# Kernel tuning notes

Hardware: AMD Instinct MI355X
Metric: run time of the kernel (lower is better)

The kernel has to match this reference:

```python
import jax, jax.numpy as jnp
import numpy as np
import math

L, D, H, V, B, S, MR = 8, 768, 12, 32000, 2, 1024, 4
HD = D // H

def setup_inputs() -> dict:
    key = jax.random.key(0)
    ks = iter(jax.random.split(key, 64))
    def rn(shape, s=0.02):
        return jax.random.normal(next(ks), shape, jnp.float32) * s
    inp = {}
    inp['tokens'] = jax.random.randint(next(ks), (B, S), 0, V, jnp.int32)
    inp['tok_emb'] = rn((V, D))
    inp['pos_emb'] = rn((S, D))
    for n in ['Wq_row', 'Wk_row', 'Wv_row', 'Wq_col', 'Wo']:
        inp[n] = rn((L, D, D))
    for n in ['bq_row', 'bk_row', 'bv_row', 'bq_col', 'bo']:
        inp[n] = jnp.zeros((L, D), jnp.float32)
    inp['ln1_g'] = jnp.ones((L, D), jnp.float32); inp['ln1_b'] = jnp.zeros((L, D), jnp.float32)
    inp['ln2_g'] = jnp.ones((L, D), jnp.float32); inp['ln2_b'] = jnp.zeros((L, D), jnp.float32)
    inp['W1'] = rn((L, D, MR * D)); inp['b1'] = jnp.zeros((L, MR * D), jnp.float32)
    inp['W2'] = rn((L, MR * D, D)); inp['b2'] = jnp.zeros((L, D), jnp.float32)
    inp['Wk_sh'] = rn((D, D)); inp['bk_sh'] = jnp.zeros((D,), jnp.float32)
    inp['Wv_sh'] = rn((D, D)); inp['bv_sh'] = jnp.zeros((D,), jnp.float32)
    inp['lnf_g'] = jnp.ones((D,), jnp.float32); inp['lnf_b'] = jnp.zeros((D,), jnp.float32)
    inp['Whead'] = rn((D, V)); inp['bhead'] = jnp.zeros((V,), jnp.float32)
    return inp

def _ln(x, g, b, eps=1e-5):
    m = x.mean(-1, keepdims=True)
    v = ((x - m) ** 2).mean(-1, keepdims=True)
    return (x - m) * jax.lax.rsqrt(v + eps) * g + b

def _heads(x):
    b, s, _ = x.shape
    return x.reshape(b, s, H, HD).transpose(0, 2, 1, 3)  # [B,H,S,hd]

def _merge(x):
    b, h, s, hd = x.shape
    return x.transpose(0, 2, 1, 3).reshape(b, s, h * hd)

def _forward(tokens, tok_emb, pos_emb, Wq_row, bq_row, Wk_row, bk_row, Wv_row, bv_row,
             Wq_col, bq_col, Wo, bo, ln1_g, ln1_b, ln2_g, ln2_b, W1, b1, W2, b2,
             Wk_sh, bk_sh, Wv_sh, bv_sh, lnf_g, lnf_b, Whead, bhead):
    s_len = tokens.shape[1]
    inv = 1.0 / math.sqrt(HD)
    x = tok_emb[tokens] + pos_emb[:s_len]
    mask = jnp.triu(jnp.ones((s_len, s_len), bool), 1)
    past_k, past_v = [], []
    for i in range(L):
        h = _ln(x, ln1_g[i], ln1_b[i])
        q_row = _heads(h @ Wq_row[i] + bq_row[i])
        k_row = _heads(h @ Wk_row[i] + bk_row[i])
        v_row = _heads(h @ Wv_row[i] + bv_row[i])
        q_col = _heads(h @ Wq_col[i] + bq_col[i])
        k_col = _heads(h @ Wk_sh + bk_sh)   # shared KV projector (archived memory)
        v_col = _heads(h @ Wv_sh + bv_sh)
        ts = jnp.einsum('bhqd,bhkd->bhqk', q_row, k_row) * inv
        ts = jnp.where(mask, -jnp.inf, ts)
        if past_k:
            pk = jnp.stack(past_k, axis=3)  # [B,H,S,l,hd]
            pv = jnp.stack(past_v, axis=3)
            ms = jnp.einsum('bhsd,bhsld->bhsl', q_col, pk) * inv
            w = jax.nn.softmax(jnp.concatenate([ts, ms], axis=-1), axis=-1)
            tw, mw = w[..., :s_len], w[..., s_len:]
            ctx = (jnp.einsum('bhqk,bhkd->bhqd', tw, v_row)
                   + jnp.einsum('bhsl,bhsld->bhsd', mw, pv))
        else:
            ctx = jnp.einsum('bhqk,bhkd->bhqd', jax.nn.softmax(ts, axis=-1), v_row)
        x = x + (_merge(ctx) @ Wo[i] + bo[i])
        h2 = _ln(x, ln2_g[i], ln2_b[i])
        x = x + (jax.nn.gelu(h2 @ W1[i] + b1[i], approximate=False) @ W2[i] + b2[i])
        past_k.append(k_col)
        past_v.append(v_col)
    return _ln(x, lnf_g, lnf_b) @ Whead + bhead

def reference(tokens, tok_emb, pos_emb, Wq_row, bq_row, Wk_row, bk_row, Wv_row, bv_row,
              Wq_col, bq_col, Wo, bo, ln1_g, ln1_b, ln2_g, ln2_b, W1, b1, W2, b2,
              Wk_sh, bk_sh, Wv_sh, bv_sh, lnf_g, lnf_b, Whead, bhead):
    return _forward(tokens, tok_emb, pos_emb, Wq_row, bq_row, Wk_row, bk_row, Wv_row, bv_row,
                    Wq_col, bq_col, Wo, bo, ln1_g, ln1_b, ln2_g, ln2_b, W1, b1, W2, b2,
                    Wk_sh, bk_sh, Wv_sh, bv_sh, lnf_g, lnf_b, Whead, bhead)
```

## Files before the change

### kernel.cpp

```cpp
#include <hip/hip_runtime.h>
#include <hip/hip_bf16.h>
#include <math.h>

#define L_   8
#define D_   768
#define H_   12
#define V_   32000
#define B_   2
#define S_   1024
#define HD_  64
#define BS_  2048
#define DFF_ 3072

typedef __hip_bfloat16 bf16;
typedef __attribute__((ext_vector_type(8))) short bf16x8;
typedef __attribute__((ext_vector_type(4))) float f32x4;

#define CFUN(r) (((r) >> 1) & 3)

__device__ __forceinline__ void cp16(void* lds, const void* g) {
  __builtin_amdgcn_global_load_lds(
      (const __attribute__((address_space(1))) void*)g,
      (__attribute__((address_space(3))) void*)lds, 16, 0, 0);
}

__device__ __forceinline__ unsigned short f2bf(float v) {
  __hip_bfloat16 h = __float2bfloat16(v);
  return *reinterpret_cast<unsigned short*>(&h);
}
__device__ __forceinline__ float bf2f(unsigned short u) {
  return __uint_as_float(((unsigned)u) << 16);
}

__global__ __launch_bounds__(256) void k_embed(const int* __restrict__ tokens,
    const float* __restrict__ tok_emb, const float* __restrict__ pos_emb,
    float* __restrict__ x) {
  int idx = blockIdx.x * 256 + threadIdx.x;
  int row = idx / D_;
  int d   = idx - row * D_;
  int s   = row & (S_ - 1);
  int t   = tokens[row];
  x[idx] = tok_emb[(size_t)t * D_ + d] + pos_emb[(size_t)s * D_ + d];
}

__global__ __launch_bounds__(256) void k_ln(const float* __restrict__ x,
    const float* __restrict__ g, const float* __restrict__ b,
    bf16* __restrict__ out) {
  int row = blockIdx.x;
  const float* xr = x + (size_t)row * D_;
  int t = threadIdx.x;
  float v0 = xr[t], v1 = xr[t + 256], v2 = xr[t + 512];
  float s  = v0 + v1 + v2;
  float s2 = v0 * v0 + v1 * v1 + v2 * v2;
#pragma unroll
  for (int off = 32; off; off >>= 1) {
    s  += __shfl_down(s, off);
    s2 += __shfl_down(s2, off);
  }
  __shared__ float rs[4], rs2[4];
  __shared__ float mean_s, rstd_s;
  int wid = t >> 6;
  if ((t & 63) == 0) { rs[wid] = s; rs2[wid] = s2; }
  __syncthreads();
  if (t == 0) {
    float S1 = rs[0] + rs[1] + rs[2] + rs[3];
    float S2 = rs2[0] + rs2[1] + rs2[2] + rs2[3];
    float m  = S1 / D_;
    float var = S2 / D_ - m * m;
    mean_s = m;
    rstd_s = rsqrtf(var + 1e-5f);
  }
  __syncthreads();
  float m = mean_s, r = rstd_s;
  bf16* orow = out + (size_t)row * D_;
  orow[t]       = __float2bfloat16((v0 - m) * r * g[t]       + b[t]);
  orow[t + 256] = __float2bfloat16((v1 - m) * r * g[t + 256] + b[t + 256]);
  orow[t + 512] = __float2bfloat16((v2 - m) * r * g[t + 512] + b[t + 512]);
}

__global__ __launch_bounds__(256) void k_w2bf_t(const float* __restrict__ W,
    bf16* __restrict__ Wt, int K, int N, size_t ils, size_t ols) {
  __shared__ float t[32][33];
  const float* Wm = W + (size_t)blockIdx.z * ils;
  bf16* Wtm = Wt + (size_t)blockIdx.z * ols;
  int n0 = blockIdx.x * 32, k0 = blockIdx.y * 32;
  int tx = threadIdx.x;
  for (int i = threadIdx.y; i < 32; i += 8)
    t[i][tx] = Wm[(size_t)(k0 + i) * N + n0 + tx];
  __syncthreads();
  for (int i = threadIdx.y; i < 32; i += 8)
    Wtm[(size_t)(n0 + i) * K + k0 + tx] = __float2bfloat16(t[tx][i]);
}

__global__ __launch_bounds__(256) void k_bcat(const float* __restrict__ bq,
    const float* __restrict__ bk, const float* __restrict__ bqc,
    const float* __restrict__ bv, const float* __restrict__ bksh,
    const float* __restrict__ bvsh, float* __restrict__ b6) {
  int idx = blockIdx.x * 256 + threadIdx.x;
  if (idx >= L_ * 4608) return;
  int l = idx / 4608, c = idx - l * 4608;
  float v = (c < 768)  ? bq[l * 768 + c]
          : (c < 1536) ? bk[l * 768 + c - 768]
          : (c < 2304) ? bqc[l * 768 + c - 1536]
          : (c < 3072) ? bv[l * 768 + c - 2304]
          : (c < 3840) ? bksh[c - 3072]
                       : bvsh[c - 3840];
  b6[idx] = v;
}

template <int BM, int EPI>
__global__ __launch_bounds__(256) void k_bgemm(
    const bf16* __restrict__ A, const bf16* __restrict__ Wt,
    const float* __restrict__ bias, const float* __restrict__ resid,
    float* __restrict__ Cf, bf16* __restrict__ Cb, bf16* __restrict__ Cb2,
    bf16* __restrict__ Cb3, int NM, int M, int N, int K) {
  constexpr int ASZ = BM * 64;
  constexpr int ALINES = BM / 64;
  constexpr int BSTRIDE = ASZ + 8192;
  constexpr int MF = BM / 32;
  __shared__ __align__(16) char smem[3 * BSTRIDE];
  const int tid = threadIdx.x;
  const int l = tid & 63, w = tid >> 6;
  const int wr = w >> 1, wc = w & 1;

  const int nwg = (int)gridDim.x;
  int id = (int)blockIdx.x;
  id = (id & 7) * (nwg >> 3) + (id >> 3);
  const int m0 = (id % NM) * BM;
  const int n0 = (id / NM) * 128;

  const int lane15 = l & 15, lg = l >> 4;

  const int r0 = tid >> 2, p0 = tid & 3;
  const char* aSrc[ALINES];
#pragma unroll
  for (int i = 0; i < ALINES; i++) {
    const int rr = i * 64 + r0;
    aSrc[i] = (const char*)(A + (size_t)(m0 + rr) * K) + ((p0 ^ CFUN(rr)) * 16);
  }
  const char* bSrc0 = (const char*)(Wt + (size_t)(n0 + r0) * K) + ((p0 ^ CFUN(r0)) * 16);
  const char* bSrc1 = (const char*)(Wt + (size_t)(n0 + 64 + r0) * K) + ((p0 ^ CFUN(64 + r0)) * 16);

  int aOff[MF], bOff[4];
#pragma unroll
  for (int mi = 0; mi < MF; mi++) {
    int r = wr * (BM / 2) + mi * 16 + lane15;
    aOff[mi] = r * 64 + ((lg ^ CFUN(r)) * 16);
  }
#pragma unroll
  for (int ni = 0; ni < 4; ni++) {
    int r = wc * 64 + ni * 16 + lane15;
    bOff[ni] = ASZ + r * 64 + ((lg ^ CFUN(r)) * 16);
  }

  f32x4 acc[MF][4];
#pragma unroll
  for (int mi = 0; mi < MF; mi++)
#pragma unroll
    for (int ni = 0; ni < 4; ni++) acc[mi][ni] = (f32x4){0.f, 0.f, 0.f, 0.f};

  auto stage = [&](int buf, int t) {
    const size_t kb = (size_t)t * 64;
    char* base = smem + buf * BSTRIDE;
#pragma unroll
    for (int i = 0; i < ALINES; i++)
      cp16(base + i * 4096 + w * 1024, aSrc[i] + kb);
    cp16(base + ASZ + w * 1024, bSrc0 + kb);
    cp16(base + ASZ + 4096 + w * 1024, bSrc1 + kb);
  };
  auto compute = [&](int buf) {
    const char* base = smem + buf * BSTRIDE;
    bf16x8 af[MF], bfr[4];
#pragma unroll
    for (int mi = 0; mi < MF; mi++) af[mi] = *(const bf16x8*)(base + aOff[mi]);
#pragma unroll
    for (int ni = 0; ni < 4; ni++) bfr[ni] = *(const bf16x8*)(base + bOff[ni]);
    __builtin_amdgcn_s_setprio(1);
#pragma unroll
    for (int mi = 0; mi < MF; mi++)
#pragma unroll
      for (int ni = 0; ni < 4; ni++)
        acc[mi][ni] = __builtin_amdgcn_mfma_f32_16x16x32_bf16(
            af[mi], bfr[ni], acc[mi][ni], 0, 0, 0);
    __builtin_amdgcn_s_setprio(0);
  };

  const int nk = K >> 5;
  stage(0, 0);
  stage(1, 1);
  int buf = 0;
  for (int t = 0; t < nk; t++) {
    if (t + 1 < nk) {
      if constexpr (ALINES == 2) asm volatile("s_waitcnt vmcnt(4)" ::: "memory");
      else                       asm volatile("s_waitcnt vmcnt(3)" ::: "memory");
    } else {
      asm volatile("s_waitcnt vmcnt(0)" ::: "memory");
    }
    __builtin_amdgcn_s_barrier();
    if (t + 2 < nk) {
      int nb = buf + 2; if (nb >= 3) nb -= 3;
      stage(nb, t + 2);
    }
    compute(buf);
    buf = (buf == 2) ? 0 : buf + 1;
  }

#pragma unroll
  for (int ni = 0; ni < 4; ni++) {
    const int col = n0 + wc * 64 + ni * 16 + lane15;
    const float bv = bias[col];
#pragma unroll
    for (int mi = 0; mi < MF; mi++) {
      const int rowb = m0 + wr * (BM / 2) + mi * 16 + lg * 4;
      if constexpr (EPI == 6) {
        if (col < 2304) {
#pragma unroll
          for (int j = 0; j < 4; j++)
            Cb[(size_t)(rowb + j) * 2304 + col] = __float2bfloat16(acc[mi][ni][j] + bv);
        } else if (col < 3072) {
          ushort4 pk;
          pk.x = f2bf(acc[mi][ni][0] + bv);
          pk.y = f2bf(acc[mi][ni][1] + bv);
          pk.z = f2bf(acc[mi][ni][2] + bv);
          pk.w = f2bf(acc[mi][ni][3] + bv);
          const int bq = rowb >> 10, s = rowb & (S_ - 1);
          *reinterpret_cast<ushort4*>(
              (unsigned short*)Cb2 + ((size_t)(bq * 768 + (col - 2304))) * S_ + s) = pk;
        } else {
#pragma unroll
          for (int j = 0; j < 4; j++)
            Cb3[(size_t)(rowb + j) * 1536 + (col - 3072)] =
                __float2bfloat16(acc[mi][ni][j] + bv);
        }
      } else {
#pragma unroll
        for (int j = 0; j < 4; j++) {
          const int row = rowb + j;
          float v = acc[mi][ni][j] + bv;
          if constexpr (EPI == 1) v += resid[(size_t)row * N + col];
          if constexpr (EPI == 2) {
            v = 0.5f * v * (1.0f + erff(v * 0.70710678118654752f));
            Cb[(size_t)row * N + col] = __float2bfloat16(v);
          } else if constexpr (EPI == 3) {
            Cb[(size_t)row * N + col] = __float2bfloat16(v);
          } else {
            Cf[(size_t)row * N + col] = v;
          }
        }
      }
    }
  }
}

#define HBAR() asm volatile("s_barrier" ::: "memory")
#define MFMA16(AF, BF, MB, NB)                                               \
  do {                                                                       \
    __builtin_amdgcn_s_setprio(1);                                           \
    _Pragma("unroll") for (int mi_ = 0; mi_ < 4; mi_++)                      \
      _Pragma("unroll") for (int ni_ = 0; ni_ < 2; ni_++)                    \
        _Pragma("unroll") for (int ks_ = 0; ks_ < 2; ks_++)                  \
          acc[(MB) + mi_][(NB) + ni_] =                                      \
              __builtin_amdgcn_mfma_f32_16x16x32_bf16(                       \
                  AF[mi_][ks_], BF[ni_][ks_], acc[(MB) + mi_][(NB) + ni_],   \
                  0, 0, 0);                                                  \
    __builtin_amdgcn_s_setprio(0);                                           \
  } while (0)

__global__ __launch_bounds__(512, 1) void k_head8(const bf16* __restrict__ A,
    const bf16* __restrict__ Wt, const float* __restrict__ bias,
    float* __restrict__ C) {
  __shared__ __align__(16) char smem[131072];
  const int tid = threadIdx.x;
  const int l = tid & 63, w = tid >> 6;
  const int wr = w >> 2, wc = w & 3;
  const int lane15 = l & 15, lg = l >> 4;

  int id = (int)blockIdx.x;
  id = (id & 7) * 125 + (id >> 3);
  const int m0 = (id % 8) * 256;
  const int n0 = (id / 8) * 256;

  auto issueA = [&](int tile, int hb) {
#pragma unroll
    for (int j = 0; j < 2; j++) {
      const int idx = j * 512 + tid;
      const int rl = idx >> 3, sl = idx & 7;
      const bf16* g = A + (size_t)(m0 + hb + rl) * 768 + tile * 64 +
                      ((sl ^ (rl & 7)) << 3);
      cp16(smem + (tile & 1) * 32768 + hb * 128 + (j * 512 + w * 64) * 16, g);
    }
  };
  auto issueB = [&](int tile, int hb) {
#pragma unroll
    for (int j = 0; j < 2; j++) {
      const int idx = j * 512 + tid;
      const int rl = idx >> 3, sl = idx & 7;
      const bf16* g = Wt + (size_t)(n0 + hb + rl) * 768 + tile * 64 +
                      ((sl ^ (rl & 7)) << 3);
      cp16(smem + 65536 + (tile & 1) * 32768 + hb * 128 + (j * 512 + w * 64) * 16, g);
    }
  };
  auto ldA = [&](int buf, int mi, int ks) {
    const int r = wr * 128 + mi * 16 + lane15;
    return *(const bf16x8*)(smem + buf * 32768 + r * 128 +
                            ((((ks << 2) + lg) ^ (r & 7)) << 4));
  };
  auto ldB = [&](int buf, int ni, int ks) {
    const int r = wc * 64 + ni * 16 + lane15;
    return *(const bf16x8*)(smem + 65536 + buf * 32768 + r * 128 +
                            ((((ks << 2) + lg) ^ (r & 7)) << 4));
  };

  f32x4 acc[8][4];
#pragma unroll
  for (int i = 0; i < 8; i++)
#pragma unroll
    for (int j = 0; j < 4; j++) acc[i][j] = (f32x4){0.f, 0.f, 0.f, 0.f};
  bf16x8 alo[4][2], ahi[4][2], blo[2][2], bhi[2][2];

  issueA(0, 0);  issueA(0, 128);  issueB(0, 0);  issueB(0, 128);
  issueB(1, 0);  issueA(1, 0);    issueB(1, 128);
  asm volatile("s_waitcnt vmcnt(6)" ::: "memory");
  HBAR();

  for (int it = 0; it < 5; ++it) {
    const int Tb = 2 * it + 1, Tn = 2 * it + 2;
#pragma unroll
    for (int mi = 0; mi < 4; mi++) { alo[mi][0] = ldA(0, mi, 0); alo[mi][1] = ldA(0, mi, 1); }
#pragma unroll
    for (int ni = 0; ni < 2; ni++) { blo[ni][0] = ldB(0, ni, 0); blo[ni][1] = ldB(0, ni, 1); }
    issueA(Tb, 128);
    HBAR(); MFMA16(alo, blo, 0, 0); HBAR();
#pragma unroll
    for (int ni = 0; ni < 2; ni++) { bhi[ni][0] = ldB(0, ni + 2, 0); bhi[ni][1] = ldB(0, ni + 2, 1); }
    HBAR(); MFMA16(alo, bhi, 0, 2); HBAR();
#pragma unroll
    for (int mi = 0; mi < 4; mi++) { ahi[mi][0] = ldA(0, mi + 4, 0); ahi[mi][1] = ldA(0, mi + 4, 1); }
    issueB(Tn, 0);
    HBAR(); MFMA16(ahi, bhi, 4, 2); HBAR();
    issueA(Tn, 0);
    issueB(Tn, 128);
    asm volatile("s_waitcnt vmcnt(6)" ::: "memory");
    HBAR(); MFMA16(ahi, blo, 4, 0); HBAR();
#pragma unroll
    for (int mi = 0; mi < 4; mi++) { alo[mi][0] = ldA(1, mi, 0); alo[mi][1] = ldA(1, mi, 1); }
#pragma unroll
    for (int ni = 0; ni < 2; ni++) { blo[ni][0] = ldB(1, ni, 0); blo[ni][1] = ldB(1, ni, 1); }
    issueA(Tn, 128);
    HBAR(); MFMA16(alo, blo, 0, 0); HBAR();
#pragma unroll
    for (int ni = 0; ni < 2; ni++) { bhi[ni][0] = ldB(1, ni + 2, 0); bhi[ni][1] = ldB(1, ni + 2, 1); }
    HBAR(); MFMA16(alo, bhi, 0, 2); HBAR();
#pragma unroll
    for (int mi = 0; mi < 4; mi++) { ahi[mi][0] = ldA(1, mi + 4, 0); ahi[mi][1] = ldA(1, mi + 4, 1); }
    issueB(Tn + 1, 0);
    HBAR(); MFMA16(ahi, bhi, 4, 2); HBAR();
    issueA(Tn + 1, 0);
    issueB(Tn + 1, 128);
    asm volatile("s_waitcnt vmcnt(6)" ::: "memory");
    HBAR(); MFMA16(ahi, blo, 4, 0); HBAR();
  }

  {
#pragma unroll
    for (int mi = 0; mi < 4; mi++) { alo[mi][0] = ldA(0, mi, 0); alo[mi][1] = ldA(0, mi, 1); }
#pragma unroll
    for (int ni = 0; ni < 2; ni++) { blo[ni][0] = ldB(0, ni, 0); blo[ni][1] = ldB(0, ni, 1); }
    issueA(11, 128);
    HBAR(); MFMA16(alo, blo, 0, 0); HBAR();
#pragma unroll
    for (int ni = 0; ni < 2; ni++) { bhi[ni][0] = ldB(0, ni + 2, 0); bhi[ni][1] = ldB(0, ni + 2, 1); }
    HBAR(); MFMA16(alo, bhi, 0, 2); HBAR();
#pragma unroll
    for (int mi = 0; mi < 4; mi++) { ahi[mi][0] = ldA(0, mi + 4, 0); ahi[mi][1] = ldA(0, mi + 4, 1); }
    HBAR(); MFMA16(ahi, bhi, 4, 2); HBAR();
    asm volatile("s_waitcnt vmcnt(0)" ::: "memory");
    HBAR(); MFMA16(ahi, blo, 4, 0); HBAR();
#pragma unroll
    for (int mi = 0; mi < 4; mi++) { alo[mi][0] = ldA(1, mi, 0); alo[mi][1] = ldA(1, mi, 1); }
#pragma unroll
    for (int ni = 0; ni < 2; ni++) { blo[ni][0] = ldB(1, ni, 0); blo[ni][1] = ldB(1, ni, 1); }
    MFMA16(alo, blo, 0, 0);
#pragma unroll
    for (int ni = 0; ni < 2; ni++) { bhi[ni][0] = ldB(1, ni + 2, 0); bhi[ni][1] = ldB(1, ni + 2, 1); }
    MFMA16(alo, bhi, 0, 2);
#pragma unroll
    for (int mi = 0; mi < 4; mi++) { ahi[mi][0] = ldA(1, mi + 4, 0); ahi[mi][1] = ldA(1, mi + 4, 1); }
    MFMA16(ahi, bhi, 4, 2);
    MFMA16(ahi, blo, 4, 0);
  }

#pragma unroll
  for (int ni = 0; ni < 4; ni++) {
    const int col = n0 + wc * 64 + ni * 16 + lane15;
    const float bv = bias[col];
#pragma unroll
    for (int mi = 0; mi < 8; mi++) {
      const int rowb = m0 + wr * 128 + mi * 16 + lg * 4;
#pragma unroll
      for (int j = 0; j < 4; j++)
        C[(size_t)(rowb + j) * 32000 + col] = acc[mi][ni][j] + bv;
    }
  }
}

__global__ __launch_bounds__(256) void k_attn(
    const bf16* __restrict__ qkv, const bf16* __restrict__ vT,
    const bf16* __restrict__ memkv, bf16* __restrict__ ctx, int layer) {
  const int bh = blockIdx.x;
  const int b = bh / H_, h = bh % H_;
  const int qt = (int)gridDim.y - 1 - (int)blockIdx.y;
  const int tid = threadIdx.x;
  const int w = tid >> 6, l = tid & 63;
  const int lane15 = l & 15, lg = l >> 4;
  const float inv = 0.125f;

  __shared__ char plds[4][2048];
  __shared__ float wlp[4][16][16];
  char* pl = plds[w];

  const int qrow0 = qt * 64 + w * 16;
  const size_t rowA = (size_t)(b * S_ + qrow0 + lane15);
  const bf16* qp = qkv + rowA * 2304 + h * 64 + lg * 8;
  const bf16x8 qf0 = *(const bf16x8*)(qp);
  const bf16x8 qf1 = *(const bf16x8*)(qp + 32);

  const bf16* kbase = qkv + (size_t)(b * S_) * 2304 + 768 + h * 64 + lg * 8;
  const bf16* vbase = vT + ((size_t)(b * 768 + h * 64 + lane15)) * S_;

  float mrow[4], dsum[4];
  f32x4 acc[4];
#pragma unroll
  for (int j = 0; j < 4; j++) { mrow[j] = -INFINITY; dsum[j] = 0.f; }
#pragma unroll
  for (int ni = 0; ni < 4; ni++) acc[ni] = (f32x4){0.f, 0.f, 0.f, 0.f};

  const int ntile = ((qrow0 + 15) >> 6) + 1;
  for (int kt64 = 0; kt64 < ntile; kt64++) {
    const int k0 = kt64 * 64;
    f32x4 sc[4];
#pragma unroll
    for (int kt = 0; kt < 4; kt++) {
      const bf16* kp = kbase + (size_t)(k0 + kt * 16 + lane15) * 2304;
      bf16x8 kf0 = *(const bf16x8*)(kp);
      bf16x8 kf1 = *(const bf16x8*)(kp + 32);
      f32x4 z = (f32x4){0.f, 0.f, 0.f, 0.f};
      z = __builtin_amdgcn_mfma_f32_16x16x32_bf16(qf0, kf0, z, 0, 0, 0);
      sc[kt] = __builtin_amdgcn_mfma_f32_16x16x32_bf16(qf1, kf1, z, 0, 0, 0);
    }
    float tmax[4];
#pragma unroll
    for (int j = 0; j < 4; j++) tmax[j] = -INFINITY;
#pragma unroll
    for (int kt = 0; kt < 4; kt++) {
      const int kabs = k0 + kt * 16 + lane15;
#pragma unroll
      for (int j = 0; j < 4; j++) {
        const int qabs = qrow0 + lg * 4 + j;
        float v = (kabs <= qabs) ? sc[kt][j] * inv : -INFINITY;
        sc[kt][j] = v;
        tmax[j] = fmaxf(tmax[j], v);
      }
    }
#pragma unroll
    for (int off = 1; off < 16; off <<= 1)
#pragma unroll
      for (int j = 0; j < 4; j++) tmax[j] = fmaxf(tmax[j], __shfl_xor(tmax[j], off, 16));

    float psum[4];
#pragma unroll
    for (int j = 0; j < 4; j++) {
      const float mnew = fmaxf(mrow[j], tmax[j]);
      const float alpha = __expf(mrow[j] - mnew);
      mrow[j] = mnew;
      dsum[j] *= alpha;
#pragma unroll
      for (int ni = 0; ni < 4; ni++) acc[ni][j] *= alpha;
      psum[j] = 0.f;
    }
#pragma unroll
    for (int kt = 0; kt < 4; kt++) {
      const int gsl = kt * 2 + (lane15 >> 3);
      const int ebyte = (lane15 & 7) * 2;
#pragma unroll
      for (int j = 0; j < 4; j++) {
        const float p = __expf(sc[kt][j] - mrow[j]);
        psum[j] += p;
        const int r = lg * 4 + j;
        *(unsigned short*)(pl + r * 128 + ((gsl ^ (r & 7)) << 4) + ebyte) = f2bf(p);
      }
    }
#pragma unroll
    for (int off = 1; off < 16; off <<= 1)
#pragma unroll
      for (int j = 0; j < 4; j++) psum[j] += __shfl_xor(psum[j], off, 16);
#pragma unroll
    for (int j = 0; j < 4; j++) dsum[j] += psum[j];

#pragma unroll
    for (int ks = 0; ks < 2; ks++) {
      bf16x8 pa = *(const bf16x8*)(pl + lane15 * 128 +
                                   ((((ks << 2) + lg) ^ (lane15 & 7)) << 4));
      const bf16* vp = vbase + k0 + ks * 32 + lg * 8;
#pragma unroll
      for (int ni = 0; ni < 4; ni++) {
        bf16x8 vf = *(const bf16x8*)(vp + (size_t)ni * 16 * S_);
        acc[ni] = __builtin_amdgcn_mfma_f32_16x16x32_bf16(pa, vf, acc[ni], 0, 0, 0);
      }
    }
  }

  const int r4 = lg * 4;
  if (lane15 < layer) {
    const int ml = lane15;
#pragma unroll
    for (int j = 0; j < 4; j++) {
      const size_t rowB = (size_t)(b * S_) + qrow0 + r4 + j;
      const bf16* qc = qkv + rowB * 2304 + 1536 + h * 64;
      const bf16* mk = memkv + ((size_t)ml * BS_ + rowB) * 1536 + h * 64;
      float d_ = 0.f;
#pragma unroll
      for (int t = 0; t < 8; t++) {
        bf16x8 qv = *(const bf16x8*)(qc + t * 8);
        bf16x8 kv = *(const bf16x8*)(mk + t * 8);
#pragma unroll
        for (int e = 0; e < 8; e++)
          d_ += bf2f((unsigned short)qv[e]) * bf2f((unsigned short)kv[e]);
      }
      wlp[w][r4 + j][ml] = d_ * inv;
    }
  }
  if (layer > 0) {
#pragma unroll
    for (int j = 0; j < 4; j++) {
      const int r = r4 + j;
      float mm = -INFINITY;
      for (int ml = 0; ml < layer; ml++) mm = fmaxf(mm, wlp[w][r][ml]);
      const float mnew = fmaxf(mrow[j], mm);
      const float alpha = __expf(mrow[j] - mnew);
      mrow[j] = mnew;
      dsum[j] *= alpha;
#pragma unroll
      for (int ni = 0; ni < 4; ni++) acc[ni][j] *= alpha;
      const size_t rowB = (size_t)(b * S_) + qrow0 + r;
      for (int ml = 0; ml < layer; ml++) {
        const float p = __expf(wlp[w][r][ml] - mnew);
        dsum[j] += p;
        const unsigned short* mv = (const unsigned short*)(memkv +
            ((size_t)ml * BS_ + rowB) * 1536 + 768 + h * 64 + lane15);
#pragma unroll
        for (int ni = 0; ni < 4; ni++)
          acc[ni][j] += p * bf2f(mv[ni * 16]);
      }
    }
  }

#pragma unroll
  for (int j = 0; j < 4; j++) {
    const float rd = 1.f / dsum[j];
    const size_t rowB = (size_t)(b * S_) + qrow0 + r4 + j;
    bf16* cp = ctx + rowB * 768 + h * 64 + lane15;
#pragma unroll
    for (int ni = 0; ni < 4; ni++)
      cp[ni * 16] = __float2bfloat16(acc[ni][j] * rd);
  }
}

extern "C" void kernel_launch(void* const* d_in, const int* in_sizes, int n_in,
                              void* d_out, int out_size, void* d_ws, size_t ws_size,
                              hipStream_t stream) {
  const int*   tokens  = (const int*)d_in[0];
  const float* tok_emb = (const float*)d_in[1];
  const float* pos_emb = (const float*)d_in[2];
  const float *Wq_row, *Wk_row, *Wv_row, *Wq_col, *Wo;
  const float *bq_row, *bk_row, *bv_row, *bq_col, *bo;
  if (in_sizes[4] == L_ * D_ * D_) {
    Wq_row = (const float*)d_in[3];  Wk_row = (const float*)d_in[4];
    Wv_row = (const float*)d_in[5];  Wq_col = (const float*)d_in[6];
    Wo     = (const float*)d_in[7];
    bq_row = (const float*)d_in[8];  bk_row = (const float*)d_in[9];
    bv_row = (const float*)d_in[10]; bq_col = (const float*)d_in[11];
    bo     = (const float*)d_in[12];
  } else {
    Wq_row = (const float*)d_in[3];  bq_row = (const float*)d_in[4];
    Wk_row = (const float*)d_in[5];  bk_row = (const float*)d_in[6];
    Wv_row = (const float*)d_in[7];  bv_row = (const float*)d_in[8];
    Wq_col = (const float*)d_in[9];  bq_col = (const float*)d_in[10];
    Wo     = (const float*)d_in[11]; bo     = (const float*)d_in[12];
  }
  const float* ln1_g = (const float*)d_in[13]; const float* ln1_b = (const float*)d_in[14];
  const float* ln2_g = (const float*)d_in[15]; const float* ln2_b = (const float*)d_in[16];
  const float* W1    = (const float*)d_in[17]; const float* b1    = (const float*)d_in[18];
  const float* W2    = (const float*)d_in[19]; const float* b2    = (const float*)d_in[20];
  const float* Wk_sh = (const float*)d_in[21]; const float* bk_sh = (const float*)d_in[22];
  const float* Wv_sh = (const float*)d_in[23]; const float* bv_sh = (const float*)d_in[24];
  const float* lnf_g = (const float*)d_in[25]; const float* lnf_b = (const float*)d_in[26];
  const float* Whead = (const float*)d_in[27]; const float* bhead = (const float*)d_in[28];

  char* p = (char*)d_ws;
  float* x      = (float*)p; p += (size_t)BS_ * D_ * 4;
  bf16*  h_bf   = (bf16*)p;  p += (size_t)BS_ * D_ * 2;
  bf16*  qkv3   = (bf16*)p;  p += (size_t)BS_ * 2304 * 2;
  bf16*  vTb    = (bf16*)p;  p += (size_t)B_ * 768 * S_ * 2;
  bf16*  memkv  = (bf16*)p;  p += (size_t)L_ * BS_ * 1536 * 2;
  bf16*  ctx_bf = (bf16*)p;  p += (size_t)BS_ * D_ * 2;
  bf16*  mlp_bf = (bf16*)p;  p += (size_t)BS_ * DFF_ * 2;
  float* b6cat  = (float*)p; p += (size_t)L_ * 4608 * 4;
  bf16* tW6    = (bf16*)p; p += (size_t)L_ * 4608 * D_ * 2;
  bf16* tWo    = (bf16*)p; p += (size_t)L_ * D_ * D_ * 2;
  bf16* tW1    = (bf16*)p; p += (size_t)L_ * DFF_ * D_ * 2;
  bf16* tW2    = (bf16*)p; p += (size_t)L_ * D_ * DFF_ * 2;
  bf16* tWhead = (bf16*)p; p += (size_t)V_ * D_ * 2;

  dim3 tb(32, 8);
  const size_t DD = (size_t)D_ * D_;
  const size_t W6S = (size_t)4608 * 768;
  k_w2bf_t<<<dim3(24, 24, L_), tb, 0, stream>>>(Wq_row, tW6,              768, 768, DD, W6S);
  k_w2bf_t<<<dim3(24, 24, L_), tb, 0, stream>>>(Wk_row, tW6 + 768 * 768,  768, 768, DD, W6S);
  k_w2bf_t<<<dim3(24, 24, L_), tb, 0, stream>>>(Wq_col, tW6 + 1536 * 768, 768, 768, DD, W6S);
  k_w2bf_t<<<dim3(24, 24, L_), tb, 0, stream>>>(Wv_row, tW6 + 2304 * 768, 768, 768, DD, W6S);
  k_w2bf_t<<<dim3(24, 24, L_), tb, 0, stream>>>(Wk_sh,  tW6 + 3072 * 768, 768, 768, 0, W6S);
  k_w2bf_t<<<dim3(24, 24, L_), tb, 0, stream>>>(Wv_sh,  tW6 + 3840 * 768, 768, 768, 0, W6S);
  k_w2bf_t<<<dim3(24, 24, L_), tb, 0, stream>>>(Wo,     tWo, 768, 768, DD, DD);
  k_w2bf_t<<<dim3(96, 24, L_), tb, 0, stream>>>(W1, tW1, 768, 3072, (size_t)768 * 3072, (size_t)3072 * 768);
  k_w2bf_t<<<dim3(24, 96, L_), tb, 0, stream>>>(W2, tW2, 3072, 768, (size_t)768 * 3072, (size_t)768 * 3072);
  k_w2bf_t<<<dim3(1000, 24, 1), tb, 0, stream>>>(Whead, tWhead, 768, 32000, 0, 0);
  k_bcat<<<dim3(144), 256, 0, stream>>>(bq_row, bk_row, bq_col, bv_row, bk_sh, bv_sh, b6cat);

  k_embed<<<dim3((BS_ * D_) / 256), 256, 0, stream>>>(tokens, tok_emb, pos_emb, x);

  for (int i = 0; i < L_; i++) {
    k_ln<<<dim3(BS_), 256, 0, stream>>>(x, ln1_g + i * D_, ln1_b + i * D_, h_bf);
    k_bgemm<128, 6><<<dim3(576), 256, 0, stream>>>(
        h_bf, tW6 + (size_t)i * W6S, b6cat + (size_t)i * 4608,
        nullptr, nullptr, qkv3, vTb, memkv + (size_t)i * BS_ * 1536,
        16, BS_, 4608, 768);
    k_attn<<<dim3(B_ * H_, S_ / 64), 256, 0, stream>>>(qkv3, vTb, memkv, ctx_bf, i);
    k_bgemm<64, 1><<<dim3(192), 256, 0, stream>>>(
        ctx_bf, tWo + (size_t)i * DD, bo + i * D_, x, x, nullptr, nullptr, nullptr,
        32, BS_, 768, 768);
    k_ln<<<dim3(BS_), 256, 0, stream>>>(x, ln2_g + i * D_, ln2_b + i * D_, h_bf);
    k_bgemm<128, 2><<<dim3(384), 256, 0, stream>>>(
        h_bf, tW1 + (size_t)i * 3072 * 768, b1 + (size_t)i * DFF_,
        nullptr, nullptr, mlp_bf, nullptr, nullptr, 16, BS_, 3072, 768);
    k_bgemm<64, 1><<<dim3(192), 256, 0, stream>>>(
        mlp_bf, tW2 + (size_t)i * 768 * 3072, b2 + i * D_, x, x, nullptr, nullptr,
        nullptr, 32, BS_, 768, 3072);
  }
  k_ln<<<dim3(BS_), 256, 0, stream>>>(x, lnf_g, lnf_b, h_bf);
  k_head8<<<dim3(1000), 512, 0, stream>>>(h_bf, tWhead, bhead, (float*)d_out);
}
```

Baseline: 1.844 ms.

## Split-K the W2 GEMM with a reduction kernel and dedupe shared KV weights

The second MLP GEMM (K=3072) now runs as a two-way split-K launch with 384 workgroups instead of 192, writing fp32 partial sums. A new elementwise kernel then adds both partials, the bias and the residual into x. The aim is better CU occupancy on this small-N GEMM, at the cost of an extra launch and extra fp32 traffic for the partials. Separately, the shared Wk_sh/Wv_sh weights are converted once into their own buffer and selected by column range inside the QKV GEMM, instead of being copied into every layer's weight block.

Result: faster. 1.772 ms (-3.9%).

```diff
diff --git a/kernel.cpp b/kernel.cpp
--- a/kernel.cpp
+++ b/kernel.cpp
@@ -108,9 +108,25 @@
   b6[idx] = v;
 }
 
-template <int BM, int EPI>
+__global__ __launch_bounds__(256) void k_red(float* __restrict__ x,
+    const float* __restrict__ pk, const float* __restrict__ bias, int N) {
+  const int i = (blockIdx.x * 256 + threadIdx.x) * 4;
+  const int col = i % N;
+  const size_t MN = (size_t)BS_ * N;
+  float4 a  = *reinterpret_cast<const float4*>(x + i);
+  float4 p0 = *reinterpret_cast<const float4*>(pk + i);
+  float4 p1 = *reinterpret_cast<const float4*>(pk + MN + i);
+  a.x += p0.x + p1.x + bias[col];
+  a.y += p0.y + p1.y + bias[col + 1];
+  a.z += p0.z + p1.z + bias[col + 2];
+  a.w += p0.w + p1.w + bias[col + 3];
+  *reinterpret_cast<float4*>(x + i) = a;
+}
+
+template <int BM, int EPI, int KSPL>
 __global__ __launch_bounds__(256) void k_bgemm(
     const bf16* __restrict__ A, const bf16* __restrict__ Wt,
+    const bf16* __restrict__ Wt2,
     const float* __restrict__ bias, const float* __restrict__ resid,
     float* __restrict__ Cf, bf16* __restrict__ Cb, bf16* __restrict__ Cb2,
     bf16* __restrict__ Cb3, int NM, int M, int N, int K) {
@@ -126,20 +142,33 @@
   const int nwg = (int)gridDim.x;
   int id = (int)blockIdx.x;
   id = (id & 7) * (nwg >> 3) + (id >> 3);
+  int sk = 0;
+  if constexpr (KSPL == 2) {
+    const int TT = nwg >> 1;
+    sk = id / TT;
+    id -= sk * TT;
+  }
   const int m0 = (id % NM) * BM;
   const int n0 = (id / NM) * 128;
+  const int kstart = sk * (K / KSPL);
 
   const int lane15 = l & 15, lg = l >> 4;
+
+  const bf16* WB = Wt;
+  int nb0 = n0;
+  if constexpr (EPI == 6) {
+    if (n0 >= 3072) { WB = Wt2; nb0 = n0 - 3072; }
+  }
 
   const int r0 = tid >> 2, p0 = tid & 3;
   const char* aSrc[ALINES];
 #pragma unroll
   for (int i = 0; i < ALINES; i++) {
     const int rr = i * 64 + r0;
-    aSrc[i] = (const char*)(A + (size_t)(m0 + rr) * K) + ((p0 ^ CFUN(rr)) * 16);
-  }
-  const char* bSrc0 = (const char*)(Wt + (size_t)(n0 + r0) * K) + ((p0 ^ CFUN(r0)) * 16);
-  const char* bSrc1 = (const char*)(Wt + (size_t)(n0 + 64 + r0) * K) + ((p0 ^ CFUN(64 + r0)) * 16);
+    aSrc[i] = (const char*)(A + (size_t)(m0 + rr) * K + kstart) + ((p0 ^ CFUN(rr)) * 16);
+  }
+  const char* bSrc0 = (const char*)(WB + (size_t)(nb0 + r0) * K + kstart) + ((p0 ^ CFUN(r0)) * 16);
+  const char* bSrc1 = (const char*)(WB + (size_t)(nb0 + 64 + r0) * K + kstart) + ((p0 ^ CFUN(64 + r0)) * 16);
 
   int aOff[MF], bOff[4];
 #pragma unroll
@@ -185,7 +214,7 @@
     __builtin_amdgcn_s_setprio(0);
   };
 
-  const int nk = K >> 5;
+  const int nk = (K / KSPL) >> 5;
   stage(0, 0);
   stage(1, 1);
   int buf = 0;
@@ -232,6 +261,10 @@
             Cb3[(size_t)(rowb + j) * 1536 + (col - 3072)] =
                 __float2bfloat16(acc[mi][ni][j] + bv);
         }
+      } else if constexpr (EPI == 7) {
+#pragma unroll
+        for (int j = 0; j < 4; j++)
+          Cf[(size_t)sk * M * N + (size_t)(rowb + j) * N + col] = acc[mi][ni][j];
       } else {
 #pragma unroll
         for (int j = 0; j < 4; j++) {
@@ -605,8 +638,10 @@
   bf16*  memkv  = (bf16*)p;  p += (size_t)L_ * BS_ * 1536 * 2;
   bf16*  ctx_bf = (bf16*)p;  p += (size_t)BS_ * D_ * 2;
   bf16*  mlp_bf = (bf16*)p;  p += (size_t)BS_ * DFF_ * 2;
+  float* pkbuf  = (float*)p; p += (size_t)2 * BS_ * D_ * 4;
   float* b6cat  = (float*)p; p += (size_t)L_ * 4608 * 4;
-  bf16* tW6    = (bf16*)p; p += (size_t)L_ * 4608 * D_ * 2;
+  bf16* tW6    = (bf16*)p; p += (size_t)L_ * 3072 * D_ * 2;
+  bf16* tWsh   = (bf16*)p; p += (size_t)1536 * D_ * 2;
   bf16* tWo    = (bf16*)p; p += (size_t)L_ * D_ * D_ * 2;
   bf16* tW1    = (bf16*)p; p += (size_t)L_ * DFF_ * D_ * 2;
   bf16* tW2    = (bf16*)p; p += (size_t)L_ * D_ * DFF_ * 2;
@@ -614,13 +649,13 @@
 
   dim3 tb(32, 8);
   const size_t DD = (size_t)D_ * D_;
-  const size_t W6S = (size_t)4608 * 768;
+  const size_t W6S = (size_t)3072 * 768;
   k_w2bf_t<<<dim3(24, 24, L_), tb, 0, stream>>>(Wq_row, tW6,              768, 768, DD, W6S);
   k_w2bf_t<<<dim3(24, 24, L_), tb, 0, stream>>>(Wk_row, tW6 + 768 * 768,  768, 768, DD, W6S);
   k_w2bf_t<<<dim3(24, 24, L_), tb, 0, stream>>>(Wq_col, tW6 + 1536 * 768, 768, 768, DD, W6S);
   k_w2bf_t<<<dim3(24, 24, L_), tb, 0, stream>>>(Wv_row, tW6 + 2304 * 768, 768, 768, DD, W6S);
-  k_w2bf_t<<<dim3(24, 24, L_), tb, 0, stream>>>(Wk_sh,  tW6 + 3072 * 768, 768, 768, 0, W6S);
-  k_w2bf_t<<<dim3(24, 24, L_), tb, 0, stream>>>(Wv_sh,  tW6 + 3840 * 768, 768, 768, 0, W6S);
+  k_w2bf_t<<<dim3(24, 24, 1), tb, 0, stream>>>(Wk_sh, tWsh,             768, 768, 0, 0);
+  k_w2bf_t<<<dim3(24, 24, 1), tb, 0, stream>>>(Wv_sh, tWsh + 768 * 768, 768, 768, 0, 0);
   k_w2bf_t<<<dim3(24, 24, L_), tb, 0, stream>>>(Wo,     tWo, 768, 768, DD, DD);
   k_w2bf_t<<<dim3(96, 24, L_), tb, 0, stream>>>(W1, tW1, 768, 3072, (size_t)768 * 3072, (size_t)3072 * 768);
   k_w2bf_t<<<dim3(24, 96, L_), tb, 0, stream>>>(W2, tW2, 3072, 768, (size_t)768 * 3072, (size_t)768 * 3072);
@@ -631,21 +666,22 @@
 
   for (int i = 0; i < L_; i++) {
     k_ln<<<dim3(BS_), 256, 0, stream>>>(x, ln1_g + i * D_, ln1_b + i * D_, h_bf);
-    k_bgemm<128, 6><<<dim3(576), 256, 0, stream>>>(
-        h_bf, tW6 + (size_t)i * W6S, b6cat + (size_t)i * 4608,
+    k_bgemm<128, 6, 1><<<dim3(576), 256, 0, stream>>>(
+        h_bf, tW6 + (size_t)i * W6S, tWsh, b6cat + (size_t)i * 4608,
         nullptr, nullptr, qkv3, vTb, memkv + (size_t)i * BS_ * 1536,
         16, BS_, 4608, 768);
     k_attn<<<dim3(B_ * H_, S_ / 64), 256, 0, stream>>>(qkv3, vTb, memkv, ctx_bf, i);
-    k_bgemm<64, 1><<<dim3(192), 256, 0, stream>>>(
-        ctx_bf, tWo + (size_t)i * DD, bo + i * D_, x, x, nullptr, nullptr, nullptr,
-        32, BS_, 768, 768);
+    k_bgemm<64, 1, 1><<<dim3(192), 256, 0, stream>>>(
+        ctx_bf, tWo + (size_t)i * DD, nullptr, bo + i * D_, x, x,
+        nullptr, nullptr, nullptr, 32, BS_, 768, 768);
     k_ln<<<dim3(BS_), 256, 0, stream>>>(x, ln2_g + i * D_, ln2_b + i * D_, h_bf);
-    k_bgemm<128, 2><<<dim3(384), 256, 0, stream>>>(
-        h_bf, tW1 + (size_t)i * 3072 * 768, b1 + (size_t)i * DFF_,
+    k_bgemm<128, 2, 1><<<dim3(384), 256, 0, stream>>>(
+        h_bf, tW1 + (size_t)i * 3072 * 768, nullptr, b1 + (size_t)i * DFF_,
         nullptr, nullptr, mlp_bf, nullptr, nullptr, 16, BS_, 3072, 768);
-    k_bgemm<64, 1><<<dim3(192), 256, 0, stream>>>(
-        mlp_bf, tW2 + (size_t)i * 768 * 3072, b2 + i * D_, x, x, nullptr, nullptr,
-        nullptr, 32, BS_, 768, 3072);
+    k_bgemm<64, 7, 2><<<dim3(384), 256, 0, stream>>>(
+        mlp_bf, tW2 + (size_t)i * 768 * 3072, nullptr, b2 + i * D_,
+        nullptr, pkbuf, nullptr, nullptr, nullptr, 32, BS_, 768, 3072);
+    k_red<<<dim3((BS_ * D_) / 1024), 256, 0, stream>>>(x, pkbuf, b2 + i * D_, D_);
   }
   k_ln<<<dim3(BS_), 256, 0, stream>>>(x, lnf_g, lnf_b, h_bf);
   k_head8<<<dim3(1000), 512, 0, stream>>>(h_bf, tWhead, bhead, (float*)d_out);
```
